# Kernel tuning notes

Hardware: AMD Instinct MI355X
Metric: run time of the kernel (lower is better)

## Reference

```python
import jax, jax.numpy as jnp
import numpy as np

B, C, E = 2, 128, 60000

def conv1(x, W, b):
    # pointwise conv1d: x [B,Cin,E], W [Cout,Cin], b [Cout] -> [B,Cout,E]
    return jnp.einsum('oc,bce->boe', W, x) + b[None, :, None]

def mesh_conv(x, gi, W, b):
    # MeshCNN GeMM conv: x [B,C,E], gi [B,E,4] neighbor edge ids, W [Cout,Cin,5], b [Cout]
    f = jax.vmap(lambda xb, ib: xb[:, ib])(x, gi)  # [B,C,E,4] neighbor gather
    f1, f2, f3, f4 = f[..., 0], f[..., 1], f[..., 2], f[..., 3]
    # symmetric features: [e, a+c, b+d, |a-c|, |b-d|]
    G = jnp.stack([x, f1 + f3, f2 + f4, jnp.abs(f1 - f3), jnp.abs(f2 - f4)], axis=-1)  # [B,C,E,5]
    return jnp.einsum('bces,ocs->boe', G, W) + b[None, :, None]


def setup_inputs() -> dict:
    key = jax.random.key(0)
    ks = jax.random.split(key, 16)
    s = 0.05
    return {
        'x_0': jax.random.normal(ks[0], (B, C, E), jnp.float32),
        'x_1': jax.random.normal(ks[1], (B, C, E), jnp.float32),
        'gemm': jax.random.randint(ks[2], (B, E, 4), 0, E, jnp.int32),
        'Wa_local': jax.random.normal(ks[3], (C, C), jnp.float32) * s,
        'ba_local': jax.random.normal(ks[4], (C,), jnp.float32) * s,
        'Wb_local': jax.random.normal(ks[5], (C, C), jnp.float32) * s,
        'bb_local': jax.random.normal(ks[6], (C,), jnp.float32) * s,
        'Wa_tri': jax.random.normal(ks[7], (C, C, 5), jnp.float32) * s,
        'ba_tri': jax.random.normal(ks[8], (C,), jnp.float32) * s,
        'Wb_tri': jax.random.normal(ks[9], (C, C, 5), jnp.float32) * s,
        'bb_tri': jax.random.normal(ks[10], (C,), jnp.float32) * s,
        'Wa_fuse': jax.random.normal(ks[11], (3, 2 * C), jnp.float32) * s,
        'ba_fuse': jax.random.normal(ks[12], (3,), jnp.float32) * s,
        'Wb_fuse': jax.random.normal(ks[13], (3, 2 * C), jnp.float32) * s,
        'bb_fuse': jax.random.normal(ks[14], (3,), jnp.float32) * s,
    }


def reference(x_0, x_1, gemm, Wa_local, ba_local, Wb_local, bb_local,
              Wa_tri, ba_tri, Wb_tri, bb_tri,
              Wa_fuse, ba_fuse, Wb_fuse, bb_fuse):
    a_local = conv1(x_0, Wa_local, ba_local)              # [B,C,E]
    a_tri = mesh_conv(x_0, gemm, Wa_tri, ba_tri)          # [B,C,E]
    x_a_two = jnp.concatenate([a_local, a_tri], axis=1)   # [B,2C,E]
    b_local = conv1(x_1, Wb_local, bb_local)
    b_tri = mesh_conv(x_1, gemm, Wb_tri, bb_tri)
    x_b_two = jnp.concatenate([b_local, b_tri], axis=1)
    x_a_w = conv1(x_a_two, Wa_fuse, ba_fuse)[:, None]     # [B,1,3,E]
    x_b_w = conv1(x_b_two, Wb_fuse, bb_fuse)[:, None]     # [B,1,3,E]
    return x_a_w + x_b_w
```

## Files before the change

### kernel.cpp

```cpp
#include <hip/hip_runtime.h>
#include <hip/hip_bf16.h>
#include <cstdint>

#define B_ 2
#define C_ 128
#define E_ 60000

typedef unsigned int uint32_;
typedef unsigned short ushort_;

__device__ __forceinline__ float2 bpair(uint32_ v) {
    union { uint32_ u; float f; } lo, hi;
    lo.u = v << 16;
    hi.u = v & 0xffff0000u;
    return make_float2(lo.f, hi.f);
}

__device__ __forceinline__ ushort_ f2b(float f) {
    union { float f; uint32_ u; } x; x.f = f;
    uint32_ u = x.u + 0x7fffu + ((x.u >> 16) & 1u);
    return (ushort_)(u >> 16);
}

__global__ __launch_bounds__(256) void fuse_weights_kernel(
    const float* __restrict__ Wa_local, const float* __restrict__ ba_local,
    const float* __restrict__ Wb_local, const float* __restrict__ bb_local,
    const float* __restrict__ Wa_tri,  const float* __restrict__ ba_tri,
    const float* __restrict__ Wb_tri,  const float* __restrict__ bb_tri,
    const float* __restrict__ Wa_fuse, const float* __restrict__ ba_fuse,
    const float* __restrict__ Wb_fuse, const float* __restrict__ bb_fuse,
    float* __restrict__ Vw, float* __restrict__ cst)
{
    int t = blockIdx.x * 256 + threadIdx.x;
    if (t < 2 * 3 * 5 * C_) {
        int c = t & (C_ - 1);
        int r = t >> 7;
        int s = r % 5; r /= 5;
        int j = r % 3;
        int p = r / 3;
        const float* Wf = p ? Wb_fuse : Wa_fuse;
        const float* Wt = p ? Wb_tri  : Wa_tri;
        const float* Wl = p ? Wb_local : Wa_local;
        float acc = 0.f;
        for (int o = 0; o < C_; ++o)
            acc += Wf[j * 256 + 128 + o] * Wt[(o * C_ + c) * 5 + s];
        if (s == 0)
            for (int o = 0; o < C_; ++o)
                acc += Wf[j * 256 + o] * Wl[o * C_ + c];
        Vw[t] = acc;
    } else if (t < 2 * 3 * 5 * C_ + 3) {
        int j = t - 2 * 3 * 5 * C_;
        float acc = ba_fuse[j] + bb_fuse[j];
        for (int o = 0; o < C_; ++o) {
            acc += Wa_fuse[j * 256 + o]       * ba_local[o]
                 + Wa_fuse[j * 256 + 128 + o] * ba_tri[o]
                 + Wb_fuse[j * 256 + o]       * bb_local[o]
                 + Wb_fuse[j * 256 + 128 + o] * bb_tri[o];
        }
        cst[j] = acc;
    }
}

__global__ __launch_bounds__(256) void transpose_bf16_kernel(
    const float* __restrict__ x0, const float* __restrict__ x1,
    ushort_* __restrict__ x0t, ushort_* __restrict__ x1t)
{
    __shared__ float tile[32][33];
    const int which = blockIdx.z >> 1;
    const int b     = blockIdx.z & 1;
    const float* src = (which ? x1 : x0) + (size_t)b * C_ * E_;
    ushort_*     dst = (which ? x1t : x0t) + (size_t)b * E_ * C_;
    const int e0 = blockIdx.x * 32;
    const int c0 = blockIdx.y * 32;
    const int t  = threadIdx.x;
    {
        const int c = t >> 3, e4 = (t & 7) * 4;
        float4 v = *(const float4*)(src + (size_t)(c0 + c) * E_ + e0 + e4);
        tile[c][e4]     = v.x;
        tile[c][e4 + 1] = v.y;
        tile[c][e4 + 2] = v.z;
        tile[c][e4 + 3] = v.w;
    }
    __syncthreads();
    {
        const int e = t >> 3, c4 = (t & 7) * 4;
        ushort4 w;
        w.x = f2b(tile[c4][e]);
        w.y = f2b(tile[c4 + 1][e]);
        w.z = f2b(tile[c4 + 2][e]);
        w.w = f2b(tile[c4 + 3][e]);
        *(ushort4*)(dst + (size_t)(e0 + e) * C_ + c0 + c4) = w;
    }
}

__global__ __launch_bounds__(256) void mesh_fused_kernel(
    const ushort_* __restrict__ x0t, const ushort_* __restrict__ x1t,
    const int* __restrict__ gemm, const float* __restrict__ Vw,
    const float* __restrict__ cst, float* __restrict__ out)
{
    const int lane = threadIdx.x & 63;
    const int wv   = threadIdx.x >> 6;
    const int gw   = blockIdx.x * 4 + wv;
    const int nw   = gridDim.x * 4;
    const int co   = lane * 2;

    float2 w[2][3][5];
#pragma unroll
    for (int p = 0; p < 2; ++p)
#pragma unroll
        for (int j = 0; j < 3; ++j)
#pragma unroll
            for (int s = 0; s < 5; ++s)
                w[p][j][s] = *(const float2*)(Vw + (((p * 3 + j) * 5 + s) << 7) + co);
    const float c0 = cst[0], c1 = cst[1], c2 = cst[2];

    for (int edge = gw; edge < B_ * E_; edge += nw) {
        const int b = edge >= E_;
        const int e = edge - b * E_;
        const int4 gi = *(const int4*)(gemm + (edge << 2));
        const ushort_* xa = x0t + (size_t)b * E_ * C_;
        const ushort_* xb = x1t + (size_t)b * E_ * C_;

        uint32_ va0 = *(const uint32_*)(xa + (e    << 7) + co);
        uint32_ va1 = *(const uint32_*)(xa + (gi.x << 7) + co);
        uint32_ va2 = *(const uint32_*)(xa + (gi.y << 7) + co);
        uint32_ va3 = *(const uint32_*)(xa + (gi.z << 7) + co);
        uint32_ va4 = *(const uint32_*)(xa + (gi.w << 7) + co);
        uint32_ vb0 = *(const uint32_*)(xb + (e    << 7) + co);
        uint32_ vb1 = *(const uint32_*)(xb + (gi.x << 7) + co);
        uint32_ vb2 = *(const uint32_*)(xb + (gi.y << 7) + co);
        uint32_ vb3 = *(const uint32_*)(xb + (gi.z << 7) + co);
        uint32_ vb4 = *(const uint32_*)(xb + (gi.w << 7) + co);

        float2 a0 = bpair(va0), a1 = bpair(va1), a2 = bpair(va2),
               a3 = bpair(va3), a4 = bpair(va4);
        float2 b0 = bpair(vb0), b1 = bpair(vb1), b2 = bpair(vb2),
               b3 = bpair(vb3), b4 = bpair(vb4);

        float2 sa1 = {a1.x + a3.x, a1.y + a3.y};
        float2 sa2 = {a2.x + a4.x, a2.y + a4.y};
        float2 da1 = {fabsf(a1.x - a3.x), fabsf(a1.y - a3.y)};
        float2 da2 = {fabsf(a2.x - a4.x), fabsf(a2.y - a4.y)};
        float2 sb1 = {b1.x + b3.x, b1.y + b3.y};
        float2 sb2 = {b2.x + b4.x, b2.y + b4.y};
        float2 db1 = {fabsf(b1.x - b3.x), fabsf(b1.y - b3.y)};
        float2 db2 = {fabsf(b2.x - b4.x), fabsf(b2.y - b4.y)};

        float acc[3];
#pragma unroll
        for (int j = 0; j < 3; ++j) {
            float t;
            t  = w[0][j][0].x * a0.x  + w[0][j][0].y * a0.y;
            t += w[0][j][1].x * sa1.x + w[0][j][1].y * sa1.y;
            t += w[0][j][2].x * sa2.x + w[0][j][2].y * sa2.y;
            t += w[0][j][3].x * da1.x + w[0][j][3].y * da1.y;
            t += w[0][j][4].x * da2.x + w[0][j][4].y * da2.y;
            t += w[1][j][0].x * b0.x  + w[1][j][0].y * b0.y;
            t += w[1][j][1].x * sb1.x + w[1][j][1].y * sb1.y;
            t += w[1][j][2].x * sb2.x + w[1][j][2].y * sb2.y;
            t += w[1][j][3].x * db1.x + w[1][j][3].y * db1.y;
            t += w[1][j][4].x * db2.x + w[1][j][4].y * db2.y;
            acc[j] = t;
        }

#pragma unroll
        for (int off = 32; off > 0; off >>= 1) {
            acc[0] += __shfl_xor(acc[0], off, 64);
            acc[1] += __shfl_xor(acc[1], off, 64);
            acc[2] += __shfl_xor(acc[2], off, 64);
        }

        if (lane == 0) {
            float* o = out + (size_t)b * 3 * E_ + e;
            o[0]      = acc[0] + c0;
            o[E_]     = acc[1] + c1;
            o[2 * E_] = acc[2] + c2;
        }
    }
}

extern "C" void kernel_launch(void* const* d_in, const int* in_sizes, int n_in,
                              void* d_out, int out_size, void* d_ws, size_t ws_size,
                              hipStream_t stream) {
    const float* x0       = (const float*)d_in[0];
    const float* x1       = (const float*)d_in[1];
    const int*   gemm     = (const int*)d_in[2];
    const float* Wa_local = (const float*)d_in[3];
    const float* ba_local = (const float*)d_in[4];
    const float* Wb_local = (const float*)d_in[5];
    const float* bb_local = (const float*)d_in[6];
    const float* Wa_tri   = (const float*)d_in[7];
    const float* ba_tri   = (const float*)d_in[8];
    const float* Wb_tri   = (const float*)d_in[9];
    const float* bb_tri   = (const float*)d_in[10];
    const float* Wa_fuse  = (const float*)d_in[11];
    const float* ba_fuse  = (const float*)d_in[12];
    const float* Wb_fuse  = (const float*)d_in[13];
    const float* bb_fuse  = (const float*)d_in[14];
    float* out = (float*)d_out;

    ushort_* x0t = (ushort_*)d_ws;
    ushort_* x1t = x0t + (size_t)B_ * E_ * C_;
    float*   Vw  = (float*)(x1t + (size_t)B_ * E_ * C_);
    float*   cst = Vw + 2 * 3 * 5 * C_;

    hipLaunchKernelGGL(fuse_weights_kernel, dim3(16), dim3(256), 0, stream,
                       Wa_local, ba_local, Wb_local, bb_local,
                       Wa_tri, ba_tri, Wb_tri, bb_tri,
                       Wa_fuse, ba_fuse, Wb_fuse, bb_fuse, Vw, cst);

    hipLaunchKernelGGL(transpose_bf16_kernel, dim3(E_ / 32, C_ / 32, 2 * B_),
                       dim3(256), 0, stream, x0, x1, x0t, x1t);

    hipLaunchKernelGGL(mesh_fused_kernel, dim3(2048), dim3(256), 0, stream,
                       x0t, x1t, gemm, Vw, cst, out);
}
```

Measured before the change: 244.9 us.

## Rework transpose tiling, reduction swizzles, packed math and index prefetch in mesh kernel

The transpose now handles 64-channel tiles with wider loads and 16-byte bf16 stores. The main kernel uses packed two-wide float vectors and prefetches the next edge's neighbor indices. Its wave reduction is restructured into ds_swizzle steps plus one cross-half shuffle, with the three outputs distributed across lane groups. The weight-fusion kernel is unrolled into four accumulators. Together these aim to cut reduction latency, per-edge instruction count and transpose overhead, at the cost of more complex reduction logic and added register pressure under launch bounds of 4.

After: 240.6 us. Within noise of the previous version (-1.8%).

```diff
diff --git a/kernel.cpp b/kernel.cpp
--- a/kernel.cpp
+++ b/kernel.cpp
@@ -8,18 +8,33 @@
 
 typedef unsigned int uint32_;
 typedef unsigned short ushort_;
-
-__device__ __forceinline__ float2 bpair(uint32_ v) {
-    union { uint32_ u; float f; } lo, hi;
-    lo.u = v << 16;
-    hi.u = v & 0xffff0000u;
-    return make_float2(lo.f, hi.f);
+typedef float v2f __attribute__((ext_vector_type(2)));
+
+__device__ __forceinline__ v2f bp2(uint32_ v) {
+    v2f r;
+    r.x = __uint_as_float(v << 16);
+    r.y = __uint_as_float(v & 0xffff0000u);
+    return r;
+}
+
+__device__ __forceinline__ v2f vabs2(v2f a) {
+    v2f r; r.x = fabsf(a.x); r.y = fabsf(a.y); return r;
 }
 
 __device__ __forceinline__ ushort_ f2b(float f) {
     union { float f; uint32_ u; } x; x.f = f;
     uint32_ u = x.u + 0x7fffu + ((x.u >> 16) & 1u);
     return (ushort_)(u >> 16);
+}
+
+__device__ __forceinline__ float swz_add(float v, const int pat) {
+    switch (pat) {
+    case 1:  return v + __int_as_float(__builtin_amdgcn_ds_swizzle(__float_as_int(v), 0x041F));
+    case 2:  return v + __int_as_float(__builtin_amdgcn_ds_swizzle(__float_as_int(v), 0x081F));
+    case 4:  return v + __int_as_float(__builtin_amdgcn_ds_swizzle(__float_as_int(v), 0x101F));
+    case 8:  return v + __int_as_float(__builtin_amdgcn_ds_swizzle(__float_as_int(v), 0x201F));
+    default: return v + __int_as_float(__builtin_amdgcn_ds_swizzle(__float_as_int(v), 0x401F));
+    }
 }
 
 __global__ __launch_bounds__(256) void fuse_weights_kernel(
@@ -41,13 +56,22 @@
         const float* Wf = p ? Wb_fuse : Wa_fuse;
         const float* Wt = p ? Wb_tri  : Wa_tri;
         const float* Wl = p ? Wb_local : Wa_local;
-        float acc = 0.f;
-        for (int o = 0; o < C_; ++o)
-            acc += Wf[j * 256 + 128 + o] * Wt[(o * C_ + c) * 5 + s];
-        if (s == 0)
-            for (int o = 0; o < C_; ++o)
-                acc += Wf[j * 256 + o] * Wl[o * C_ + c];
-        Vw[t] = acc;
+        float a0 = 0.f, a1 = 0.f, a2 = 0.f, a3 = 0.f;
+        for (int o = 0; o < C_; o += 4) {
+            a0 += Wf[j * 256 + 128 + o]     * Wt[((o)     * C_ + c) * 5 + s];
+            a1 += Wf[j * 256 + 128 + o + 1] * Wt[((o + 1) * C_ + c) * 5 + s];
+            a2 += Wf[j * 256 + 128 + o + 2] * Wt[((o + 2) * C_ + c) * 5 + s];
+            a3 += Wf[j * 256 + 128 + o + 3] * Wt[((o + 3) * C_ + c) * 5 + s];
+        }
+        if (s == 0) {
+            for (int o = 0; o < C_; o += 4) {
+                a0 += Wf[j * 256 + o]     * Wl[(o)     * C_ + c];
+                a1 += Wf[j * 256 + o + 1] * Wl[(o + 1) * C_ + c];
+                a2 += Wf[j * 256 + o + 2] * Wl[(o + 2) * C_ + c];
+                a3 += Wf[j * 256 + o + 3] * Wl[(o + 3) * C_ + c];
+            }
+        }
+        Vw[t] = (a0 + a1) + (a2 + a3);
     } else if (t < 2 * 3 * 5 * C_ + 3) {
         int j = t - 2 * 3 * 5 * C_;
         float acc = ba_fuse[j] + bb_fuse[j];
@@ -65,36 +89,41 @@
     const float* __restrict__ x0, const float* __restrict__ x1,
     ushort_* __restrict__ x0t, ushort_* __restrict__ x1t)
 {
-    __shared__ float tile[32][33];
+    __shared__ float tile[32][65];
     const int which = blockIdx.z >> 1;
     const int b     = blockIdx.z & 1;
     const float* src = (which ? x1 : x0) + (size_t)b * C_ * E_;
     ushort_*     dst = (which ? x1t : x0t) + (size_t)b * E_ * C_;
     const int e0 = blockIdx.x * 32;
-    const int c0 = blockIdx.y * 32;
+    const int c0 = blockIdx.y * 64;
     const int t  = threadIdx.x;
     {
-        const int c = t >> 3, e4 = (t & 7) * 4;
-        float4 v = *(const float4*)(src + (size_t)(c0 + c) * E_ + e0 + e4);
-        tile[c][e4]     = v.x;
-        tile[c][e4 + 1] = v.y;
-        tile[c][e4 + 2] = v.z;
-        tile[c][e4 + 3] = v.w;
+        const int c  = t >> 2;
+        const int e8 = (t & 3) * 8;
+        const float* p = src + (size_t)(c0 + c) * E_ + e0 + e8;
+        float4 v0 = *(const float4*)p;
+        float4 v1 = *(const float4*)(p + 4);
+        tile[e8 + 0][c] = v0.x; tile[e8 + 1][c] = v0.y;
+        tile[e8 + 2][c] = v0.z; tile[e8 + 3][c] = v0.w;
+        tile[e8 + 4][c] = v1.x; tile[e8 + 5][c] = v1.y;
+        tile[e8 + 6][c] = v1.z; tile[e8 + 7][c] = v1.w;
     }
     __syncthreads();
     {
-        const int e = t >> 3, c4 = (t & 7) * 4;
-        ushort4 w;
-        w.x = f2b(tile[c4][e]);
-        w.y = f2b(tile[c4 + 1][e]);
-        w.z = f2b(tile[c4 + 2][e]);
-        w.w = f2b(tile[c4 + 3][e]);
-        *(ushort4*)(dst + (size_t)(e0 + e) * C_ + c0 + c4) = w;
-    }
-}
-
-__global__ __launch_bounds__(256) void mesh_fused_kernel(
-    const ushort_* __restrict__ x0t, const ushort_* __restrict__ x1t,
+        const int e  = t >> 3;
+        const int c8 = (t & 7) * 8;
+        const float* r = &tile[e][c8];
+        uint32_ w0 = (uint32_)f2b(r[0]) | ((uint32_)f2b(r[1]) << 16);
+        uint32_ w1 = (uint32_)f2b(r[2]) | ((uint32_)f2b(r[3]) << 16);
+        uint32_ w2 = (uint32_)f2b(r[4]) | ((uint32_)f2b(r[5]) << 16);
+        uint32_ w3 = (uint32_)f2b(r[6]) | ((uint32_)f2b(r[7]) << 16);
+        uint4 w; w.x = w0; w.y = w1; w.z = w2; w.w = w3;
+        *(uint4*)(dst + (size_t)(e0 + e) * C_ + c0 + c8) = w;
+    }
+}
+
+__global__ __launch_bounds__(256, 4) void mesh_fused_kernel(
+    const uint32_* __restrict__ x0t, const uint32_* __restrict__ x1t,
     const int* __restrict__ gemm, const float* __restrict__ Vw,
     const float* __restrict__ cst, float* __restrict__ out)
 {
@@ -102,80 +131,85 @@
     const int wv   = threadIdx.x >> 6;
     const int gw   = blockIdx.x * 4 + wv;
     const int nw   = gridDim.x * 4;
-    const int co   = lane * 2;
-
-    float2 w[2][3][5];
+
+    v2f w[2][3][5];
 #pragma unroll
     for (int p = 0; p < 2; ++p)
 #pragma unroll
         for (int j = 0; j < 3; ++j)
 #pragma unroll
             for (int s = 0; s < 5; ++s)
-                w[p][j][s] = *(const float2*)(Vw + (((p * 3 + j) * 5 + s) << 7) + co);
-    const float c0 = cst[0], c1 = cst[1], c2 = cst[2];
-
-    for (int edge = gw; edge < B_ * E_; edge += nw) {
-        const int b = edge >= E_;
-        const int e = edge - b * E_;
-        const int4 gi = *(const int4*)(gemm + (edge << 2));
-        const ushort_* xa = x0t + (size_t)b * E_ * C_;
-        const ushort_* xb = x1t + (size_t)b * E_ * C_;
-
-        uint32_ va0 = *(const uint32_*)(xa + (e    << 7) + co);
-        uint32_ va1 = *(const uint32_*)(xa + (gi.x << 7) + co);
-        uint32_ va2 = *(const uint32_*)(xa + (gi.y << 7) + co);
-        uint32_ va3 = *(const uint32_*)(xa + (gi.z << 7) + co);
-        uint32_ va4 = *(const uint32_*)(xa + (gi.w << 7) + co);
-        uint32_ vb0 = *(const uint32_*)(xb + (e    << 7) + co);
-        uint32_ vb1 = *(const uint32_*)(xb + (gi.x << 7) + co);
-        uint32_ vb2 = *(const uint32_*)(xb + (gi.y << 7) + co);
-        uint32_ vb3 = *(const uint32_*)(xb + (gi.z << 7) + co);
-        uint32_ vb4 = *(const uint32_*)(xb + (gi.w << 7) + co);
-
-        float2 a0 = bpair(va0), a1 = bpair(va1), a2 = bpair(va2),
-               a3 = bpair(va3), a4 = bpair(va4);
-        float2 b0 = bpair(vb0), b1 = bpair(vb1), b2 = bpair(vb2),
-               b3 = bpair(vb3), b4 = bpair(vb4);
-
-        float2 sa1 = {a1.x + a3.x, a1.y + a3.y};
-        float2 sa2 = {a2.x + a4.x, a2.y + a4.y};
-        float2 da1 = {fabsf(a1.x - a3.x), fabsf(a1.y - a3.y)};
-        float2 da2 = {fabsf(a2.x - a4.x), fabsf(a2.y - a4.y)};
-        float2 sb1 = {b1.x + b3.x, b1.y + b3.y};
-        float2 sb2 = {b2.x + b4.x, b2.y + b4.y};
-        float2 db1 = {fabsf(b1.x - b3.x), fabsf(b1.y - b3.y)};
-        float2 db2 = {fabsf(b2.x - b4.x), fabsf(b2.y - b4.y)};
-
-        float acc[3];
-#pragma unroll
-        for (int j = 0; j < 3; ++j) {
-            float t;
-            t  = w[0][j][0].x * a0.x  + w[0][j][0].y * a0.y;
-            t += w[0][j][1].x * sa1.x + w[0][j][1].y * sa1.y;
-            t += w[0][j][2].x * sa2.x + w[0][j][2].y * sa2.y;
-            t += w[0][j][3].x * da1.x + w[0][j][3].y * da1.y;
-            t += w[0][j][4].x * da2.x + w[0][j][4].y * da2.y;
-            t += w[1][j][0].x * b0.x  + w[1][j][0].y * b0.y;
-            t += w[1][j][1].x * sb1.x + w[1][j][1].y * sb1.y;
-            t += w[1][j][2].x * sb2.x + w[1][j][2].y * sb2.y;
-            t += w[1][j][3].x * db1.x + w[1][j][3].y * db1.y;
-            t += w[1][j][4].x * db2.x + w[1][j][4].y * db2.y;
-            acc[j] = t;
-        }
-
-#pragma unroll
-        for (int off = 32; off > 0; off >>= 1) {
-            acc[0] += __shfl_xor(acc[0], off, 64);
-            acc[1] += __shfl_xor(acc[1], off, 64);
-            acc[2] += __shfl_xor(acc[2], off, 64);
-        }
-
-        if (lane == 0) {
-            float* o = out + (size_t)b * 3 * E_ + e;
-            o[0]      = acc[0] + c0;
-            o[E_]     = acc[1] + c1;
-            o[2 * E_] = acc[2] + c2;
-        }
+                w[p][j][s] = *(const v2f*)(Vw + (((p * 3 + j) * 5 + s) << 7) + lane * 2);
+
+    const int  jj     = lane >> 4;
+    const bool is0    = (jj == 0), is1 = (jj == 1);
+    const bool writer = ((lane & 15) == 0) && (jj < 3);
+    const float cj    = is0 ? cst[0] : (is1 ? cst[1] : cst[2]);
+    float* obase      = out + (size_t)(jj < 3 ? jj : 2) * E_;
+
+    const int4* g4 = (const int4*)gemm;
+    const int total = B_ * E_;
+    int4 gi = (gw < total) ? g4[gw] : make_int4(0, 0, 0, 0);
+
+    for (int edge = gw; edge < total; edge += nw) {
+        const int nxt = edge + nw;
+        const int4 gin = (nxt < total) ? g4[nxt] : gi;
+
+        const int b = (edge >= E_) ? 1 : 0;
+        const int e = edge - (b ? E_ : 0);
+        const uint32_* xa = x0t + (size_t)b * (E_ * 64);
+        const uint32_* xb = x1t + (size_t)b * (E_ * 64);
+
+        const uint32_ o0 = ((uint32_)e    << 6) + lane;
+        const uint32_ o1 = ((uint32_)gi.x << 6) + lane;
+        const uint32_ o2 = ((uint32_)gi.y << 6) + lane;
+        const uint32_ o3 = ((uint32_)gi.z << 6) + lane;
+        const uint32_ o4 = ((uint32_)gi.w << 6) + lane;
+
+        const uint32_ va0 = xa[o0], va1 = xa[o1], va2 = xa[o2],
+                      va3 = xa[o3], va4 = xa[o4];
+        const uint32_ vb0 = xb[o0], vb1 = xb[o1], vb2 = xb[o2],
+                      vb3 = xb[o3], vb4 = xb[o4];
+
+        v2f a0 = bp2(va0), a1 = bp2(va1), a2 = bp2(va2), a3 = bp2(va3), a4 = bp2(va4);
+        v2f b0 = bp2(vb0), b1 = bp2(vb1), b2 = bp2(vb2), b3 = bp2(vb3), b4 = bp2(vb4);
+
+        v2f sa1 = a1 + a3, sa2 = a2 + a4;
+        v2f da1 = vabs2(a1 - a3), da2 = vabs2(a2 - a4);
+        v2f sb1 = b1 + b3, sb2 = b2 + b4;
+        v2f db1 = vabs2(b1 - b3), db2 = vabs2(b2 - b4);
+
+        v2f t0 = w[0][0][0] * a0;
+        v2f t1 = w[0][1][0] * a0;
+        v2f t2 = w[0][2][0] * a0;
+        t0 += w[0][0][1] * sa1; t1 += w[0][1][1] * sa1; t2 += w[0][2][1] * sa1;
+        t0 += w[0][0][2] * sa2; t1 += w[0][1][2] * sa2; t2 += w[0][2][2] * sa2;
+        t0 += w[0][0][3] * da1; t1 += w[0][1][3] * da1; t2 += w[0][2][3] * da1;
+        t0 += w[0][0][4] * da2; t1 += w[0][1][4] * da2; t2 += w[0][2][4] * da2;
+        t0 += w[1][0][0] * b0;  t1 += w[1][1][0] * b0;  t2 += w[1][2][0] * b0;
+        t0 += w[1][0][1] * sb1; t1 += w[1][1][1] * sb1; t2 += w[1][2][1] * sb1;
+        t0 += w[1][0][2] * sb2; t1 += w[1][1][2] * sb2; t2 += w[1][2][2] * sb2;
+        t0 += w[1][0][3] * db1; t1 += w[1][1][3] * db1; t2 += w[1][2][3] * db1;
+        t0 += w[1][0][4] * db2; t1 += w[1][1][4] * db2; t2 += w[1][2][4] * db2;
+
+        float r0 = t0.x + t0.y;
+        float r1 = t1.x + t1.y;
+        float r2 = t2.x + t2.y;
+
+        r0 = swz_add(r0, 16);  r0 += __shfl_xor(r0, 32, 64);
+        r1 = swz_add(r1, 16);  r1 += __shfl_xor(r1, 32, 64);
+        r2 = swz_add(r2, 16);  r2 += __shfl_xor(r2, 32, 64);
+
+        float val = is0 ? r0 : (is1 ? r1 : r2);
+        val = swz_add(val, 1);
+        val = swz_add(val, 2);
+        val = swz_add(val, 4);
+        val = swz_add(val, 8);
+
+        if (writer)
+            obase[(b ? 3 * E_ : 0) + e] = val + cj;
+
+        gi = gin;
     }
 }
 
@@ -209,9 +243,9 @@
                        Wa_tri, ba_tri, Wb_tri, bb_tri,
                        Wa_fuse, ba_fuse, Wb_fuse, bb_fuse, Vw, cst);
 
-    hipLaunchKernelGGL(transpose_bf16_kernel, dim3(E_ / 32, C_ / 32, 2 * B_),
+    hipLaunchKernelGGL(transpose_bf16_kernel, dim3(E_ / 32, C_ / 64, 2 * B_),
                        dim3(256), 0, stream, x0, x1, x0t, x1t);
 
     hipLaunchKernelGGL(mesh_fused_kernel, dim3(2048), dim3(256), 0, stream,
-                       x0t, x1t, gemm, Vw, cst, out);
-}
+                       (const uint32_*)x0t, (const uint32_*)x1t, gemm, Vw, cst, out);
+}
```
